# Performance work log

Measured on AMD Instinct MI355X. Metric: run time of the kernel, lower is better.

## Reference

```python
import jax, jax.numpy as jnp
import numpy as np
import math

D = 1024
B, S = 4, 2048


def setup_inputs() -> dict:
    key = jax.random.key(0)
    ks = jax.random.split(key, 16)
    sc = 0.02
    def lin(k, dout, din):
        kw, kb = jax.random.split(k)
        return (sc * jax.random.normal(kw, (dout, din), jnp.float32),
                sc * jax.random.normal(kb, (dout,), jnp.float32))
    Wq, bq = lin(ks[0], D, D)
    Wk, bk = lin(ks[1], D, D)
    Wv, bv = lin(ks[2], D, D)
    Wmu, bmu = lin(ks[3], D, D)
    Wlv, blv = lin(ks[4], D, D)
    Wg, bg = lin(ks[5], 1, D)
    gamma = jnp.ones((D,), jnp.float32)
    beta = jnp.zeros((D,), jnp.float32)
    x = jax.random.normal(ks[6], (B, S, D), jnp.float32)
    eps = jax.random.normal(ks[7], (B, S, D), jnp.float32)
    return dict(x=x, eps=eps, Wq=Wq, bq=bq, Wk=Wk, bk=bk, Wv=Wv, bv=bv,
                Wmu=Wmu, bmu=bmu, Wlv=Wlv, blv=blv, Wg=Wg, bg=bg,
                gamma=gamma, beta=beta)


def _layernorm(x, gamma, beta, eps=1e-5):
    mu = jnp.mean(x, axis=-1, keepdims=True)
    var = jnp.mean(jnp.square(x - mu), axis=-1, keepdims=True)
    return (x - mu) * jax.lax.rsqrt(var + eps) * gamma + beta


def reference(x, eps, Wq, bq, Wk, bk, Wv, bv, Wmu, bmu, Wlv, blv, Wg, bg, gamma, beta):
    d = x.shape[-1]
    Q = jnp.einsum('bsd,ed->bse', x, Wq) + bq
    K = jnp.einsum('bsd,ed->bse', x, Wk) + bk
    V = jnp.einsum('bsd,ed->bse', x, Wv) + bv
    scores = jnp.einsum('bqd,bkd->bqk', Q, K) / (math.sqrt(d) * 1.5)
    attn = jax.nn.softmax(scores, axis=-1)
    h = jnp.einsum('bqk,bkd->bqd', attn, V)
    mu = jnp.einsum('bsd,ed->bse', h, Wmu) + bmu
    logvar = jnp.einsum('bsd,ed->bse', h, Wlv) + blv
    std = jnp.exp(0.5 * logvar)
    z = jax.nn.relu(mu + eps * std)
    p_gate = jax.nn.sigmoid(jnp.einsum('bd,ed->be', h.mean(axis=1), Wg) + bg)
    out = _layernorm(x + z, gamma, beta)
    return out, mu, logvar, p_gate.squeeze(-1)
```

## Files before the change

### kernel.cpp

```cpp
#include <hip/hip_runtime.h>

typedef unsigned short u16;
typedef __attribute__((ext_vector_type(8))) short bf16x8;
typedef __attribute__((ext_vector_type(4))) float f32x4;

__device__ inline float bf2f(u16 h) {
    union { unsigned u; float f; } v; v.u = ((unsigned)h) << 16; return v.f;
}
__device__ inline u16 f2bf(float f) {
    union { float f; unsigned u; } v; v.f = f;
    unsigned r = v.u + 0x7fffu + ((v.u >> 16) & 1u);
    return (u16)(r >> 16);
}

__device__ inline void gl_lds16(const u16* g, u16* l) {
    __builtin_amdgcn_global_load_lds(
        (const __attribute__((address_space(1))) void*)g,
        (__attribute__((address_space(3))) void*)l, 16, 0, 0);
}

__device__ __forceinline__ void wgbar() {
    asm volatile("" ::: "memory");
    __builtin_amdgcn_s_barrier();
    asm volatile("" ::: "memory");
}
#define VMW(n) asm volatile("s_waitcnt vmcnt(" #n ")" ::: "memory")

__global__ __launch_bounds__(256) void cvt_bf16_k(
    const float* __restrict__ s0, u16* __restrict__ d0, long long n0,
    const float* __restrict__ s1, u16* __restrict__ d1, long long n1,
    const float* __restrict__ s2, u16* __restrict__ d2, long long n2,
    const float* __restrict__ s3, u16* __restrict__ d3, long long n3)
{
    int y = blockIdx.y;
    const float* s = (y == 0) ? s0 : (y == 1) ? s1 : (y == 2) ? s2 : s3;
    u16* d         = (y == 0) ? d0 : (y == 1) ? d1 : (y == 2) ? d2 : d3;
    long long n    = (y == 0) ? n0 : (y == 1) ? n1 : (y == 2) ? n2 : n3;
    for (long long i = (long long)blockIdx.x * 256 + threadIdx.x; i < n;
         i += (long long)gridDim.x * 256) {
        float4 v = ((const float4*)s)[i];
        union { u16 h[4]; unsigned long long u; } p;
        p.h[0] = f2bf(v.x); p.h[1] = f2bf(v.y);
        p.h[2] = f2bf(v.z); p.h[3] = f2bf(v.w);
        ((unsigned long long*)d)[i] = p.u;
    }
}

#define OSTA(T, SL2, S)                                                       \
    { const u16* g_ = Ag + (long long)((S) * 64 + w * 16 + orow) * K          \
                      + (long long)(T) * 32 + oscol;                          \
      gl_lds16(g_, &As[(SL2) * 4096 + (S) * 2048 + w * 512]); }

#define OSTB(T, SL2, S)                                                       \
    { const u16* g_ = Bg + (long long)(bn0 + (S) * 64 + w * 16 + orow) * ldb  \
                      + (long long)(T) * 32 + oscol;                          \
      gl_lds16(g_, &Bs[(SL2) * 4096 + (S) * 2048 + w * 512]); }

template <int COUTF32, int BIASROW, int NSPLIT, int GATE>
__device__ __forceinline__ void gemm_body(
    const u16* __restrict__ A, const u16* __restrict__ Bt,
    const float* __restrict__ bias0, const float* __restrict__ bias1,
    void* __restrict__ C0, void* __restrict__ C1,
    int M, int N, int K, int ldb, float scale,
    long long sAb, long long sBb, long long sCb, long long bofs_stride,
    int bx, int by, int bz, int tid,
    const float* __restrict__ Wg, float* __restrict__ gatebuf,
    u16* lds)
{
    u16* As = lds;
    u16* Bs = lds + 12288;

    int bm0 = bx * 128;
    int bn0 = by * 128;
    int b   = bz;
    int w = tid >> 6, l = tid & 63;
    int wm = w >> 1;
    int wn = w & 1;
    int lane15 = l & 15, quad = l >> 4;
    int xr = (l & 3) << 3;

    int orow  = l >> 2;
    int oscol = ((l & 3) ^ (orow & 3)) * 8;

    const u16* Ag = A  + (long long)b * sAb + (long long)bm0 * K;
    const u16* Bg = Bt + (long long)b * sBb + (long long)(bm0 >> 11) * bofs_stride;

    f32x4 acc[4][4];
#pragma unroll
    for (int i = 0; i < 4; i++)
#pragma unroll
        for (int j = 0; j < 4; j++) acc[i][j] = (f32x4)(0.0f);

    int NT = K >> 5;

    OSTA(0, 0, 0); OSTA(0, 0, 1); OSTB(0, 0, 0); OSTB(0, 0, 1);
    OSTA(1, 1, 0); OSTA(1, 1, 1); OSTB(1, 1, 0); OSTB(1, 1, 1);
    VMW(4);
    wgbar();

    int sl = 0, sl2 = 2;
    for (int t = 0; t < NT; ++t) {
        bf16x8 av[4], bvv[4];
#pragma unroll
        for (int ii = 0; ii < 4; ii++)
            av[ii] = *(const bf16x8*)&As[sl * 4096 +
                (wm * 64 + ii * 16 + lane15) * 32 + ((quad * 8) ^ xr)];
#pragma unroll
        for (int jj = 0; jj < 4; jj++)
            bvv[jj] = *(const bf16x8*)&Bs[sl * 4096 +
                (wn * 64 + jj * 16 + lane15) * 32 + ((quad * 8) ^ xr)];

        if (t + 2 < NT) {
            int t2 = t + 2;
            OSTA(t2, sl2, 0); OSTA(t2, sl2, 1);
            OSTB(t2, sl2, 0); OSTB(t2, sl2, 1);
            VMW(4);
        } else if (t + 1 < NT) {
            VMW(0);
        }
        wgbar();

        __builtin_amdgcn_s_setprio(1);
#pragma unroll
        for (int ii = 0; ii < 4; ii++)
#pragma unroll
            for (int jj = 0; jj < 4; jj++)
                acc[ii][jj] = __builtin_amdgcn_mfma_f32_16x16x32_bf16(
                    av[ii], bvv[jj], acc[ii][jj], 0, 0, 0);
        __builtin_amdgcn_s_setprio(0);
        wgbar();

        sl  = (sl  == 2) ? 0 : sl + 1;
        sl2 = (sl2 == 2) ? 0 : sl2 + 1;
    }

    float rowb_[4][4];
    if (BIASROW) {
#pragma unroll
        for (int i = 0; i < 4; i++)
#pragma unroll
            for (int r = 0; r < 4; r++)
                rowb_[i][r] = bias0[bm0 + wm * 64 + i * 16 + quad * 4 + r];
    }
    float gsum = 0.0f;
#pragma unroll
    for (int jj = 0; jj < 4; jj++) {
        int col = bn0 + wn * 64 + jj * 16 + lane15;
        int seg, cl, cstride;
        if (NSPLIT == 1) { seg = 0; cl = col; cstride = N; }
        else             { seg = col >> 10; cl = col & 1023; cstride = 1024; }
        const float* bp = (seg == 0) ? bias0 : bias1;
        void* cb = (seg == 0) ? C0 : C1;
        u16*   c16 = (u16*)cb   + (long long)b * sCb;
        float* c32 = (float*)cb + (long long)b * sCb;
        float bvc = (!BIASROW && bp) ? bp[cl] : 0.0f;
        float wgc = GATE ? Wg[cl] : 0.0f;
#pragma unroll
        for (int i = 0; i < 4; i++) {
            int row0 = bm0 + wm * 64 + i * 16 + quad * 4;
#pragma unroll
            for (int r = 0; r < 4; r++) {
                float v = acc[i][jj][r] * scale + (BIASROW ? rowb_[i][r] : bvc);
                if (GATE) gsum += v * wgc;
                if (COUTF32) c32[(long long)(row0 + r) * cstride + cl] = v;
                else         c16[(long long)(row0 + r) * cstride + cl] = f2bf(v);
            }
        }
    }
    if (GATE) {
#pragma unroll
        for (int o = 32; o > 0; o >>= 1) gsum += __shfl_xor(gsum, o);
        float* red = (float*)lds;
        __syncthreads();
        if ((tid & 63) == 0) red[tid >> 6] = gsum;
        __syncthreads();
        if (tid == 0)
            atomicAdd(&gatebuf[bm0 >> 11],
                      red[0] + red[1] + red[2] + red[3]);
    }
}

template <int COUTF32, int BIASROW, int NSPLIT, int NFAST, int GATE>
__global__ __launch_bounds__(256, 3) void gemm_o(
    const u16* __restrict__ A, const u16* __restrict__ Bt,
    const float* __restrict__ bias0, const float* __restrict__ bias1,
    void* __restrict__ C0, void* __restrict__ C1,
    int M, int N, int K, int ldb, float scale,
    long long sAb, long long sBb, long long sCb, long long bofs_stride,
    const float* __restrict__ Wg, float* __restrict__ gatebuf)
{
    __shared__ u16 lds[24576];

    int gx = gridDim.x, gy = gridDim.y;
    int n = gx * gy * gridDim.z;
    int flat = (blockIdx.z * gy + blockIdx.y) * gx + blockIdx.x;
    int L = (flat & 7) * (n >> 3) + (flat >> 3);
    int bz = L / (gx * gy);
    int rr = L - bz * gx * gy;
    int bx, by;
    if (NFAST) { bx = rr / gy; by = rr - bx * gy; }
    else       { by = rr / gx; bx = rr - by * gx; }

    gemm_body<COUTF32, BIASROW, NSPLIT, GATE>(
        A, Bt, bias0, bias1, C0, C1, M, N, K, ldb, scale,
        sAb, sBb, sCb, bofs_stride, bx, by, bz, threadIdx.x, Wg, gatebuf, lds);
}

__global__ __launch_bounds__(256, 3) void qkv_k(
    const u16* __restrict__ xb, const u16* __restrict__ Wqb,
    const float* __restrict__ bq, const float* __restrict__ bk,
    u16* __restrict__ Q, u16* __restrict__ Kb,
    const u16* __restrict__ Wvb, const float* __restrict__ bv,
    u16* __restrict__ Vt)
{
    __shared__ u16 lds[24576];
    int flat = blockIdx.x;
    int tid = threadIdx.x;
    if (flat < 1024) {
        int L = (flat & 7) * 128 + (flat >> 3);
        int bx = L / 16, by = L - bx * 16;
        gemm_body<0, 0, 2, 0>(
            xb, Wqb, bq, bk, Q, Kb, 8192, 2048, 1024, 1024, 1.0f,
            0, 0, 0, 0, bx, by, 0, tid, nullptr, nullptr, lds);
    } else {
        int f2 = flat - 1024;
        int L = (f2 & 7) * 64 + (f2 >> 3);
        int by = L / 8, bx = L - by * 8;
        gemm_body<0, 1, 1, 0>(
            Wvb, xb, bv, nullptr, Vt, nullptr, 1024, 8192, 1024, 1024, 1.0f,
            0, 0, 0, 0, bx, by, 0, tid, nullptr, nullptr, lds);
    }
}

__global__ __launch_bounds__(256) void softmax_k(u16* __restrict__ Sc,
                                                 float* __restrict__ gatebuf)
{
    long long row = blockIdx.x;
    u16* s = Sc + row * 2048;
    int t = threadIdx.x;
    if (blockIdx.x == 0 && t < 4) gatebuf[t] = 0.0f;

    uint4 raw = *(const uint4*)(s + t * 8);
    const u16* rp = (const u16*)&raw;
    float v[8];
    float mx = -3.4e38f;
#pragma unroll
    for (int j = 0; j < 8; j++) { v[j] = bf2f(rp[j]); mx = fmaxf(mx, v[j]); }
#pragma unroll
    for (int o = 32; o > 0; o >>= 1) mx = fmaxf(mx, __shfl_xor(mx, o));
    __shared__ float redm[4];
    if ((t & 63) == 0) redm[t >> 6] = mx;
    __syncthreads();
    mx = fmaxf(fmaxf(redm[0], redm[1]), fmaxf(redm[2], redm[3]));

    float sum = 0.0f;
#pragma unroll
    for (int j = 0; j < 8; j++) { v[j] = __expf(v[j] - mx); sum += v[j]; }
#pragma unroll
    for (int o = 32; o > 0; o >>= 1) sum += __shfl_xor(sum, o);
    __shared__ float reds[4];
    if ((t & 63) == 0) reds[t >> 6] = sum;
    __syncthreads();
    sum = reds[0] + reds[1] + reds[2] + reds[3];

    float inv = 1.0f / sum;
    u16 o8[8];
#pragma unroll
    for (int j = 0; j < 8; j++) o8[j] = f2bf(v[j] * inv);
    *(uint4*)(s + t * 8) = *(const uint4*)o8;
}

__global__ __launch_bounds__(256) void epilogue_k(
    const float* __restrict__ x, const float* __restrict__ ep,
    const float* __restrict__ mu, const float* __restrict__ lv,
    const float* __restrict__ gamma, const float* __restrict__ beta,
    float* __restrict__ out, const float* __restrict__ bg,
    float* __restrict__ pg)
{
    long long base = (long long)blockIdx.x * 1024;
    int t = threadIdx.x;
    int i0 = t * 4;
    if (blockIdx.x == 0 && t < 4) {
        float v = pg[t] * (1.0f / 2048.0f) + bg[0];
        pg[t] = 1.0f / (1.0f + __expf(-v));
    }

    float4 xv = *(const float4*)&x[base + i0];
    float4 ev = *(const float4*)&ep[base + i0];
    float4 mv = *(const float4*)&mu[base + i0];
    float4 lw = *(const float4*)&lv[base + i0];

    float y[4];
    y[0] = xv.x + fmaxf(mv.x + ev.x * __expf(0.5f * lw.x), 0.0f);
    y[1] = xv.y + fmaxf(mv.y + ev.y * __expf(0.5f * lw.y), 0.0f);
    y[2] = xv.z + fmaxf(mv.z + ev.z * __expf(0.5f * lw.z), 0.0f);
    y[3] = xv.w + fmaxf(mv.w + ev.w * __expf(0.5f * lw.w), 0.0f);

    float sum = 0.0f, sq = 0.0f;
#pragma unroll
    for (int j = 0; j < 4; j++) { sum += y[j]; sq += y[j] * y[j]; }
#pragma unroll
    for (int o = 32; o > 0; o >>= 1) { sum += __shfl_xor(sum, o); sq += __shfl_xor(sq, o); }
    __shared__ float rs[4], rq[4];
    if ((t & 63) == 0) { rs[t >> 6] = sum; rq[t >> 6] = sq; }
    __syncthreads();
    sum = rs[0] + rs[1] + rs[2] + rs[3];
    sq  = rq[0] + rq[1] + rq[2] + rq[3];
    float mean = sum * (1.0f / 1024.0f);
    float var  = fmaxf(sq * (1.0f / 1024.0f) - mean * mean, 0.0f);
    float rstd = rsqrtf(var + 1e-5f);

    float4 gv = *(const float4*)&gamma[i0];
    float4 bv = *(const float4*)&beta[i0];
    float4 o;
    o.x = (y[0] - mean) * rstd * gv.x + bv.x;
    o.y = (y[1] - mean) * rstd * gv.y + bv.y;
    o.z = (y[2] - mean) * rstd * gv.z + bv.z;
    o.w = (y[3] - mean) * rstd * gv.w + bv.w;
    *(float4*)&out[base + i0] = o;
}

extern "C" void kernel_launch(void* const* d_in, const int* in_sizes, int n_in,
                              void* d_out, int out_size, void* d_ws, size_t ws_size,
                              hipStream_t stream)
{
    const float* x     = (const float*)d_in[0];
    const float* ep    = (const float*)d_in[1];
    const float* Wq    = (const float*)d_in[2];
    const float* bq    = (const float*)d_in[3];
    const float* Wk    = (const float*)d_in[4];
    const float* bk    = (const float*)d_in[5];
    const float* Wv    = (const float*)d_in[6];
    const float* bv    = (const float*)d_in[7];
    const float* Wmu   = (const float*)d_in[8];
    const float* bmu   = (const float*)d_in[9];
    const float* Wlv   = (const float*)d_in[10];
    const float* blv   = (const float*)d_in[11];
    const float* Wg    = (const float*)d_in[12];
    const float* bg    = (const float*)d_in[13];
    const float* gamma = (const float*)d_in[14];
    const float* beta  = (const float*)d_in[15];
    float* out = (float*)d_out;

    const int M = 8192;
    const int D = 1024;
    const int S = 2048;

    float* mu_out = out + 8388608LL;
    float* lv_out = out + 16777216LL;
    float* pg_out = out + 25165824LL;

    u16* xb   = (u16*)out;
    u16* Wqb  = (u16*)out + 8388608LL;
    u16* Wkb  = (u16*)out + 9437184LL;
    u16* Wvb  = (u16*)out + 10485760LL;
    u16* Sc   = (u16*)out;
    u16* Q    = (u16*)mu_out;
    u16* Kb   = (u16*)mu_out + 8388608LL;
    u16* Vt   = (u16*)lv_out;
    u16* h    = (u16*)d_ws;
    u16* Wmub = (u16*)out + 2097152LL;
    u16* Wlvb = (u16*)out + 3145728LL;

    dim3 blk(256);

    cvt_bf16_k<<<dim3(2048, 4), blk, 0, stream>>>(
        x,  xb,  2097152LL,
        Wq, Wqb, 262144LL,
        Wk, Wkb, 262144LL,
        Wv, Wvb, 262144LL);

    qkv_k<<<dim3(1536), blk, 0, stream>>>(
        xb, Wqb, bq, bk, Q, Kb, Wvb, bv, Vt);

    gemm_o<0, 0, 1, 1, 0><<<dim3(16, 16, 4), blk, 0, stream>>>(
        Q, Kb, nullptr, nullptr, Sc, nullptr,
        S, S, D, D, 1.0f / 48.0f,
        (long long)S * D, (long long)S * D, (long long)S * S, 0,
        nullptr, nullptr);

    softmax_k<<<dim3(8192), blk, 0, stream>>>(Sc, pg_out);

    gemm_o<0, 0, 1, 1, 1><<<dim3(64, 8, 1), blk, 0, stream>>>(
        Sc, Vt, nullptr, nullptr, h, nullptr,
        M, D, S, 8192, 1.0f, 0, 0, 0, 2048,
        Wg, pg_out);

    cvt_bf16_k<<<dim3(512, 2), blk, 0, stream>>>(
        Wmu, Wmub, 262144LL,
        Wlv, Wlvb, 262144LL,
        nullptr, nullptr, 0LL,
        nullptr, nullptr, 0LL);

    gemm_o<1, 0, 2, 1, 0><<<dim3(64, 16, 1), blk, 0, stream>>>(
        h, Wmub, bmu, blv, (void*)mu_out, (void*)lv_out,
        M, 2048, D, D, 1.0f, 0, 0, 0, 0,
        nullptr, nullptr);

    epilogue_k<<<dim3(8192), blk, 0, stream>>>(
        x, ep, mu_out, lv_out, gamma, beta, out, bg, pg_out);
}
```

Measured before the change: 407.4 us.

## Add 256x256 8-wave pipelined GEMM kernel for QK, QKV and mu/logvar projections

Adds a new 512-thread GEMM kernel with 256x256 output tiles, double-buffered swizzled LDS fed by direct global-to-LDS loads, and an interleaved load/MFMA schedule using setprio. It replaces the older 256-thread kernel for the Q/K projection, the QK^T scores GEMM and the mu/logvar projection. The fused qkv launch is split so V^T runs as its own launch on the old kernel. Larger tiles are meant to raise arithmetic intensity and cut global traffic, at the cost of one block per CU, fewer blocks in flight and an extra launch.

```diff
diff --git a/kernel.cpp b/kernel.cpp
--- a/kernel.cpp
+++ b/kernel.cpp
@@ -46,6 +46,141 @@
     }
 }
 
+#define PSTA(T, H)                                                            \
+    { const u16* g_ = Ag + (long long)((H) * 128 + w * 8 + srow) * K          \
+                      + (long long)(T) * 64 + scol;                           \
+      gl_lds16(g_, &As[(T) & 1][H][w * 512]);                                 \
+      gl_lds16(g_ + 64LL * K, &As[(T) & 1][H][4096 + w * 512]); }
+
+#define PSTB(T, H)                                                            \
+    { const u16* g_ = Bg + (long long)(bn0 + (H) * 128 + w * 8 + srow) * K    \
+                      + (long long)(T) * 64 + scol;                           \
+      gl_lds16(g_, &Bs[(T) & 1][H][w * 512]);                                 \
+      gl_lds16(g_ + 64LL * K, &Bs[(T) & 1][H][4096 + w * 512]); }
+
+#define PREADA(SL, MQ, KS)                                                    \
+    _Pragma("unroll")                                                         \
+    for (int ii = 0; ii < 4; ii++)                                            \
+        a_[ii] = *(const bf16x8*)&As[SL][wm2][                                \
+            (((MQ) * 64 + ii * 16 + lane15) * 64 + (KS) * 32 + quad * 8) ^ xr];
+
+#define PREADB(SL, KS, DST)                                                   \
+    _Pragma("unroll")                                                         \
+    for (int jj = 0; jj < 4; jj++)                                            \
+        DST[jj] = *(const bf16x8*)&Bs[SL][wn2 >> 1][                          \
+            (((wn2 & 1) * 64 + jj * 16 + lane15) * 64 + (KS) * 32 + quad * 8) ^ xr];
+
+#define PMMA(MQ, BV)                                                          \
+    __builtin_amdgcn_s_setprio(1);                                            \
+    _Pragma("unroll")                                                         \
+    for (int ii = 0; ii < 4; ii++)                                            \
+        _Pragma("unroll")                                                     \
+        for (int jj = 0; jj < 4; jj++)                                        \
+            acc[(MQ) * 4 + ii][jj] = __builtin_amdgcn_mfma_f32_16x16x32_bf16( \
+                a_[ii], BV[jj], acc[(MQ) * 4 + ii][jj], 0, 0, 0);             \
+    __builtin_amdgcn_s_setprio(0);
+
+template <int COUTF32, int NSPLIT>
+__global__ __launch_bounds__(512, 1) void gemm8p(
+    const u16* __restrict__ A, const u16* __restrict__ Bt,
+    const float* __restrict__ bias0, const float* __restrict__ bias1,
+    void* __restrict__ C0, void* __restrict__ C1,
+    int M, int N, int K, float scale,
+    long long sAb, long long sBb, long long sCb)
+{
+    __shared__ u16 As[2][2][8192];
+    __shared__ u16 Bs[2][2][8192];
+
+    int gx = gridDim.x, gy = gridDim.y;
+    int n = gx * gy * gridDim.z;
+    int flat = (blockIdx.z * gy + blockIdx.y) * gx + blockIdx.x;
+    int L = (flat & 7) * (n >> 3) + (flat >> 3);
+    int bz = L / (gx * gy);
+    int rr = L - bz * gx * gy;
+    int bx = rr / gy, by = rr - bx * gy;
+
+    int bm0 = bx * 256, bn0 = by * 256, b = bz;
+    int tid = threadIdx.x;
+    int w = tid >> 6, l = tid & 63;
+    int wm2 = w >> 2;
+    int wn2 = w & 3;
+    int lane15 = l & 15, quad = l >> 4;
+    int xr = (l & 7) << 3;
+
+    int srow = l >> 3;
+    int scol = ((l & 7) ^ srow) * 8;
+
+    const u16* Ag = A  + (long long)b * sAb + (long long)bm0 * K;
+    const u16* Bg = Bt + (long long)b * sBb;
+
+    f32x4 acc[8][4];
+#pragma unroll
+    for (int i = 0; i < 8; i++)
+#pragma unroll
+        for (int j = 0; j < 4; j++) acc[i][j] = (f32x4)(0.0f);
+
+    int NT  = K >> 6;
+    int NT2 = K >> 7;
+
+    PSTB(0, 0); PSTB(0, 1); PSTA(0, 0); PSTA(0, 1); PSTB(1, 0); PSTB(1, 1);
+    VMW(4);
+    wgbar();
+
+    for (int j = 0; j < NT2; ++j) {
+        int t1 = 2 * j + 1, t2 = 2 * j + 2, t3 = 2 * j + 3;
+        bool pf = (t2 < NT);
+        bf16x8 a_[4], b0_[4], b1_[4];
+
+        PREADA(0, 0, 0); PREADB(0, 0, b0_);
+        PSTA(t1, 0);
+        wgbar(); PMMA(0, b0_); wgbar();
+        PREADA(0, 0, 1); PREADB(0, 1, b1_);
+        PSTA(t1, 1);
+        wgbar(); PMMA(0, b1_); wgbar();
+        PREADA(0, 1, 0);
+        if (pf) PSTB(t2, 0);
+        wgbar(); PMMA(1, b0_); wgbar();
+        PREADA(0, 1, 1);
+        if (pf) { PSTB(t2, 1); VMW(4); } else { VMW(0); }
+        wgbar(); PMMA(1, b1_); wgbar();
+        PREADA(1, 0, 0); PREADB(1, 0, b0_);
+        if (pf) PSTA(t2, 0);
+        wgbar(); PMMA(0, b0_); wgbar();
+        PREADA(1, 0, 1); PREADB(1, 1, b1_);
+        if (pf) PSTA(t2, 1);
+        wgbar(); PMMA(0, b1_); wgbar();
+        PREADA(1, 1, 0);
+        if (pf) PSTB(t3, 0);
+        wgbar(); PMMA(1, b0_); wgbar();
+        PREADA(1, 1, 1);
+        if (pf) { PSTB(t3, 1); VMW(4); }
+        wgbar(); PMMA(1, b1_); wgbar();
+    }
+
+#pragma unroll
+    for (int jj = 0; jj < 4; jj++) {
+        int col = bn0 + wn2 * 64 + jj * 16 + lane15;
+        int seg, cl, cstride;
+        if (NSPLIT == 1) { seg = 0; cl = col; cstride = N; }
+        else             { seg = col >> 10; cl = col & 1023; cstride = 1024; }
+        const float* bp = (seg == 0) ? bias0 : bias1;
+        void* cb = (seg == 0) ? C0 : C1;
+        u16*   c16 = (u16*)cb   + (long long)b * sCb;
+        float* c32 = (float*)cb + (long long)b * sCb;
+        float bvc = bp ? bp[cl] : 0.0f;
+#pragma unroll
+        for (int i = 0; i < 8; i++) {
+            int row0 = bm0 + wm2 * 128 + i * 16 + quad * 4;
+#pragma unroll
+            for (int r = 0; r < 4; r++) {
+                float v = acc[i][jj][r] * scale + bvc;
+                if (COUTF32) c32[(long long)(row0 + r) * cstride + cl] = v;
+                else         c16[(long long)(row0 + r) * cstride + cl] = f2bf(v);
+            }
+        }
+    }
+}
+
 #define OSTA(T, SL2, S)                                                       \
     { const u16* g_ = Ag + (long long)((S) * 64 + w * 16 + orow) * K          \
                       + (long long)(T) * 32 + oscol;                          \
@@ -204,32 +339,6 @@
     gemm_body<COUTF32, BIASROW, NSPLIT, GATE>(
         A, Bt, bias0, bias1, C0, C1, M, N, K, ldb, scale,
         sAb, sBb, sCb, bofs_stride, bx, by, bz, threadIdx.x, Wg, gatebuf, lds);
-}
-
-__global__ __launch_bounds__(256, 3) void qkv_k(
-    const u16* __restrict__ xb, const u16* __restrict__ Wqb,
-    const float* __restrict__ bq, const float* __restrict__ bk,
-    u16* __restrict__ Q, u16* __restrict__ Kb,
-    const u16* __restrict__ Wvb, const float* __restrict__ bv,
-    u16* __restrict__ Vt)
-{
-    __shared__ u16 lds[24576];
-    int flat = blockIdx.x;
-    int tid = threadIdx.x;
-    if (flat < 1024) {
-        int L = (flat & 7) * 128 + (flat >> 3);
-        int bx = L / 16, by = L - bx * 16;
-        gemm_body<0, 0, 2, 0>(
-            xb, Wqb, bq, bk, Q, Kb, 8192, 2048, 1024, 1024, 1.0f,
-            0, 0, 0, 0, bx, by, 0, tid, nullptr, nullptr, lds);
-    } else {
-        int f2 = flat - 1024;
-        int L = (f2 & 7) * 64 + (f2 >> 3);
-        int by = L / 8, bx = L - by * 8;
-        gemm_body<0, 1, 1, 0>(
-            Wvb, xb, bv, nullptr, Vt, nullptr, 1024, 8192, 1024, 1024, 1.0f,
-            0, 0, 0, 0, bx, by, 0, tid, nullptr, nullptr, lds);
-    }
 }
 
 __global__ __launch_bounds__(256) void softmax_k(u16* __restrict__ Sc,
@@ -362,7 +471,7 @@
     u16* Wmub = (u16*)out + 2097152LL;
     u16* Wlvb = (u16*)out + 3145728LL;
 
-    dim3 blk(256);
+    dim3 blk(256), blk8(512);
 
     cvt_bf16_k<<<dim3(2048, 4), blk, 0, stream>>>(
         x,  xb,  2097152LL,
@@ -370,21 +479,23 @@
         Wk, Wkb, 262144LL,
         Wv, Wvb, 262144LL);
 
-    qkv_k<<<dim3(1536), blk, 0, stream>>>(
-        xb, Wqb, bq, bk, Q, Kb, Wvb, bv, Vt);
-
-    gemm_o<0, 0, 1, 1, 0><<<dim3(16, 16, 4), blk, 0, stream>>>(
+    gemm8p<0, 2><<<dim3(32, 8, 1), blk8, 0, stream>>>(
+        xb, Wqb, bq, bk, Q, Kb, M, 2048, D, 1.0f, 0, 0, 0);
+
+    gemm_o<0, 1, 1, 0, 0><<<dim3(8, 64, 1), blk, 0, stream>>>(
+        Wvb, xb, bv, nullptr, Vt, nullptr,
+        D, 8192, D, D, 1.0f, 0, 0, 0, 0, nullptr, nullptr);
+
+    gemm8p<0, 1><<<dim3(8, 8, 4), blk8, 0, stream>>>(
         Q, Kb, nullptr, nullptr, Sc, nullptr,
-        S, S, D, D, 1.0f / 48.0f,
-        (long long)S * D, (long long)S * D, (long long)S * S, 0,
-        nullptr, nullptr);
+        S, S, D, 1.0f / 48.0f,
+        (long long)S * D, (long long)S * D, (long long)S * S);
 
     softmax_k<<<dim3(8192), blk, 0, stream>>>(Sc, pg_out);
 
     gemm_o<0, 0, 1, 1, 1><<<dim3(64, 8, 1), blk, 0, stream>>>(
         Sc, Vt, nullptr, nullptr, h, nullptr,
-        M, D, S, 8192, 1.0f, 0, 0, 0, 2048,
-        Wg, pg_out);
+        M, D, S, 8192, 1.0f, 0, 0, 0, 2048, Wg, pg_out);
 
     cvt_bf16_k<<<dim3(512, 2), blk, 0, stream>>>(
         Wmu, Wmub, 262144LL,
@@ -392,10 +503,9 @@
         nullptr, nullptr, 0LL,
         nullptr, nullptr, 0LL);
 
-    gemm_o<1, 0, 2, 1, 0><<<dim3(64, 16, 1), blk, 0, stream>>>(
+    gemm8p<1, 2><<<dim3(32, 8, 1), blk8, 0, stream>>>(
         h, Wmub, bmu, blv, (void*)mu_out, (void*)lv_out,
-        M, 2048, D, D, 1.0f, 0, 0, 0, 0,
-        nullptr, nullptr);
+        M, 2048, D, 1.0f, 0, 0, 0);
 
     epilogue_k<<<dim3(8192), blk, 0, stream>>>(
         x, ep, mu_out, lv_out, gamma, beta, out, bg, pg_out);
```

Measured after the change: 411.2 us. About the same (+0.9%).
